# Kernel optimization log

Measured on AMD Instinct MI355X. Metric: run time of the kernel, lower is better.

The kernel has to match this reference:

```python
import jax, jax.numpy as jnp
import numpy as np

B, T, C, H = 4, 2048, 1024, 16
D = C // H          # head_dim = 64
FF = 2 * C          # ff_mult = 2
EPS = 1e-5


def _layernorm(x, g, b):
    mu = jnp.mean(x, axis=-1, keepdims=True)
    var = jnp.mean((x - mu) ** 2, axis=-1, keepdims=True)
    return (x - mu) * jax.lax.rsqrt(var + EPS) * g + b


def setup_inputs() -> dict:
    key = jax.random.key(0)
    ks = jax.random.split(key, 8)
    x = jax.random.normal(ks[0], (B, T, C), dtype=jnp.float32)
    perm = jax.random.permutation(ks[1], T).astype(jnp.int32)
    s_c = 1.0 / np.sqrt(C)
    s_f = 1.0 / np.sqrt(FF)
    Wqkv = jax.random.normal(ks[2], (C, 3 * C), dtype=jnp.float32) * s_c
    Wproj = jax.random.normal(ks[3], (C, C), dtype=jnp.float32) * s_c
    bproj = jnp.zeros((C,), dtype=jnp.float32)
    ln1_g = jnp.ones((C,), dtype=jnp.float32)
    ln1_b = jnp.zeros((C,), dtype=jnp.float32)
    ln2_g = jnp.ones((C,), dtype=jnp.float32)
    ln2_b = jnp.zeros((C,), dtype=jnp.float32)
    Wff1 = jax.random.normal(ks[4], (C, FF), dtype=jnp.float32) * s_c
    bff1 = jnp.zeros((FF,), dtype=jnp.float32)
    Wff2 = jax.random.normal(ks[5], (FF, C), dtype=jnp.float32) * s_f
    bff2 = jnp.zeros((C,), dtype=jnp.float32)
    return {"x": x, "perm": perm, "Wqkv": Wqkv, "Wproj": Wproj, "bproj": bproj,
            "ln1_g": ln1_g, "ln1_b": ln1_b, "ln2_g": ln2_g, "ln2_b": ln2_b,
            "Wff1": Wff1, "bff1": bff1, "Wff2": Wff2, "bff2": bff2}


def reference(x, perm, Wqkv, Wproj, bproj, ln1_g, ln1_b, ln2_g, ln2_b,
              Wff1, bff1, Wff2, bff2):
    # --- attention branch ---
    h = _layernorm(x, ln1_g, ln1_b)                       # [B,T,C]
    qkv = (h @ Wqkv).reshape(B, T, 3, H, D)
    q, k, v = qkv[:, :, 0], qkv[:, :, 1], qkv[:, :, 2]    # [B,T,H,D]
    # random-permuted causal additive mask: masked = ~tril[:, perm]
    rows = jnp.arange(T)[:, None]
    masked = perm[None, :] > rows                          # [T,T] bool
    bias = jnp.where(masked, -jnp.inf, 0.0).astype(x.dtype)
    scale = 1.0 / np.sqrt(D)
    scores = jnp.einsum('bqhd,bkhd->bhqk', q, k) * scale + bias
    attn = jax.nn.softmax(scores, axis=-1)                 # [B,H,T,T]
    y = jnp.einsum('bhqk,bkhd->bqhd', attn, v).reshape(B, T, C)
    x = x + y @ Wproj + bproj
    # --- MLP branch ---
    h2 = _layernorm(x, ln2_g, ln2_b)
    ff = jax.nn.gelu(h2 @ Wff1 + bff1, approximate=False) @ Wff2 + bff2
    return x + ff
```

## Files before the change

### kernel.cpp

```cpp
#include <hip/hip_runtime.h>
#include <math.h>

#define Bb 4
#define Tt 2048
#define Cc 1024
#define Hh 16
#define Dd 64
#define FFf 2048
#define Mrows (Bb*Tt)

typedef _Float16 f16;
typedef _Float16 half8 __attribute__((ext_vector_type(8)));
typedef _Float16 half4 __attribute__((ext_vector_type(4)));
typedef _Float16 half2 __attribute__((ext_vector_type(2)));
typedef float floatx4 __attribute__((ext_vector_type(4)));
typedef float floatx16 __attribute__((ext_vector_type(16)));

#define MFMA16(a,b,c)    __builtin_amdgcn_mfma_f32_16x16x32_f16(a,b,c,0,0,0)
#define MFMA16K16(a,b,c) __builtin_amdgcn_mfma_f32_16x16x16f16(a,b,c,0,0,0)
#define MFMA32(a,b,c)    __builtin_amdgcn_mfma_f32_32x32x16_f16(a,b,c,0,0,0)

__device__ __forceinline__ void g2l16(const void* g, void* l) {
  __builtin_amdgcn_global_load_lds((__attribute__((address_space(1))) void*)(g),
                                   (__attribute__((address_space(3))) void*)(l),
                                   16, 0, 0);
}

__device__ __forceinline__ float fast_gelu(float t) {
  const float z  = t * 0.70710678118654752f;
  const float az = fabsf(z);
  const float u  = __builtin_amdgcn_rcpf(1.0f + 0.3275911f * az);
  const float p  = u*(0.254829592f + u*(-0.284496736f + u*(1.421413741f +
                   u*(-1.453152027f + u*1.061405429f))));
  const float e  = 1.0f - p * __builtin_amdgcn_exp2f(-az*az*1.44269504089f);
  const float er = (z < 0.0f) ? -e : e;
  return 0.5f * t * (1.0f + er);
}

__global__ __launch_bounds__(256) void wt_ln_kernel(
    const float* __restrict__ Wqkv, const float* __restrict__ Wproj,
    const float* __restrict__ Wff1, const float* __restrict__ Wff2,
    f16* __restrict__ WqkvT, f16* __restrict__ WprojT,
    f16* __restrict__ Wff1T, f16* __restrict__ Wff2T,
    const float* __restrict__ x, const float* __restrict__ gam,
    const float* __restrict__ bet, f16* __restrict__ lnout,
    const int* __restrict__ perm, int* __restrict__ inv) {
  const int tid = threadIdx.x;
  if (blockIdx.x >= 16384) {
    #pragma unroll
    for (int i = tid; i < Tt; i += 256) inv[perm[i]] = i;
    return;
  }
  if (blockIdx.x < 8192) {
    __shared__ float tile[32][33];
    int idx = blockIdx.x;
    const float* W; f16* WT; int K, N, n0, k0;
    if (idx < 3072)      { W = Wqkv;  WT = WqkvT;  K = Cc;  N = 3*Cc; n0 = (idx % 96)*32; k0 = (idx / 96)*32; }
    else if (idx < 4096) { idx -= 3072; W = Wproj; WT = WprojT; K = Cc;  N = Cc;  n0 = (idx % 32)*32; k0 = (idx / 32)*32; }
    else if (idx < 6144) { idx -= 4096; W = Wff1;  WT = Wff1T;  K = Cc;  N = FFf; n0 = (idx % 64)*32; k0 = (idx / 64)*32; }
    else                 { idx -= 6144; W = Wff2;  WT = Wff2T;  K = FFf; N = Cc;  n0 = (idx % 32)*32; k0 = (idx / 32)*32; }
    const int tx = tid & 31, ty = tid >> 5;
    #pragma unroll
    for (int i = 0; i < 4; i++)
      tile[ty + 8*i][tx] = W[(size_t)(k0 + ty + 8*i) * N + n0 + tx];
    __syncthreads();
    #pragma unroll
    for (int i = 0; i < 4; i++)
      WT[(size_t)(n0 + ty + 8*i) * K + k0 + tx] = (f16)tile[tx][ty + 8*i];
  } else {
    const int row = blockIdx.x - 8192;
    const float4 v = ((const float4*)(x + (size_t)row * Cc))[tid];
    float s  = v.x + v.y + v.z + v.w;
    float ss = v.x*v.x + v.y*v.y + v.z*v.z + v.w*v.w;
    #pragma unroll
    for (int o = 32; o >= 1; o >>= 1) { s += __shfl_xor(s, o); ss += __shfl_xor(ss, o); }
    __shared__ float ps[4], pss[4];
    if ((tid & 63) == 0) { ps[tid >> 6] = s; pss[tid >> 6] = ss; }
    __syncthreads();
    s  = ps[0] + ps[1] + ps[2] + ps[3];
    ss = pss[0] + pss[1] + pss[2] + pss[3];
    const float mu   = s * (1.0f / Cc);
    const float rstd = rsqrtf(ss * (1.0f / Cc) - mu * mu + 1e-5f);
    const float4 g4 = ((const float4*)gam)[tid];
    const float4 b4 = ((const float4*)bet)[tid];
    half4 o;
    o[0] = (f16)((v.x - mu) * rstd * g4.x + b4.x);
    o[1] = (f16)((v.y - mu) * rstd * g4.y + b4.y);
    o[2] = (f16)((v.z - mu) * rstd * g4.z + b4.z);
    o[3] = (f16)((v.w - mu) * rstd * g4.w + b4.w);
    ((half4*)(lnout + (size_t)row * Cc))[tid] = o;
  }
}

__global__ __launch_bounds__(256) void ln_kernel(const float* __restrict__ x,
                                                 const float* __restrict__ gam,
                                                 const float* __restrict__ bet,
                                                 f16* __restrict__ out) {
  const int row = blockIdx.x;
  const int tid = threadIdx.x;
  const float4 v = ((const float4*)(x + (size_t)row * Cc))[tid];
  float s  = v.x + v.y + v.z + v.w;
  float ss = v.x*v.x + v.y*v.y + v.z*v.z + v.w*v.w;
  #pragma unroll
  for (int o = 32; o >= 1; o >>= 1) { s += __shfl_xor(s, o); ss += __shfl_xor(ss, o); }
  __shared__ float ps[4], pss[4];
  if ((tid & 63) == 0) { ps[tid >> 6] = s; pss[tid >> 6] = ss; }
  __syncthreads();
  s  = ps[0] + ps[1] + ps[2] + ps[3];
  ss = pss[0] + pss[1] + pss[2] + pss[3];
  const float mu   = s * (1.0f / Cc);
  const float rstd = rsqrtf(ss * (1.0f / Cc) - mu * mu + 1e-5f);
  const float4 g4 = ((const float4*)gam)[tid];
  const float4 b4 = ((const float4*)bet)[tid];
  half4 o;
  o[0] = (f16)((v.x - mu) * rstd * g4.x + b4.x);
  o[1] = (f16)((v.y - mu) * rstd * g4.y + b4.y);
  o[2] = (f16)((v.z - mu) * rstd * g4.z + b4.z);
  o[3] = (f16)((v.w - mu) * rstd * g4.w + b4.w);
  ((half4*)(out + (size_t)row * Cc))[tid] = o;
}

template <int MODE>
__device__ __forceinline__ void gemm_epilogue_tile(
    const floatx16& a, int rowBase, int col, int khalf,
    const float* __restrict__ resid, const float* __restrict__ bias,
    float* __restrict__ outF, f16* __restrict__ outH,
    f16* __restrict__ outQ, f16* __restrict__ outK, f16* __restrict__ outV) {
  if (MODE == 0) {
    const int s = col >> 10;
    const int hh = (col >> 6) & 15;
    const int d = col & 63;
    #pragma unroll
    for (int g = 0; g < 4; g++) {
      const int row0 = rowBase + 4*khalf + 8*g;
      const int bI = row0 >> 11;
      const int t0 = row0 & 2047;
      if (s == 2) {
        const size_t addr = (((size_t)(bI*Hh + hh)) * Dd + d) * Tt +
                            (t0 & ~63) + ((t0 >> 2) & 3)*16 + ((t0 >> 4) & 3)*4;
        half4 o;
        #pragma unroll
        for (int r = 0; r < 4; r++) o[r] = (f16)a[g*4 + r];
        *(half4*)&outV[addr] = o;
      } else {
        f16* dst = (s == 0) ? outQ : outK;
        const float sc = (s == 0) ? 0.18033688f : 1.0f;
        #pragma unroll
        for (int r = 0; r < 4; r++)
          dst[(((size_t)(bI*Hh + hh)) * Tt + t0 + r) * Dd + d] = (f16)(a[g*4 + r] * sc);
      }
    }
  } else {
    #pragma unroll
    for (int g = 0; g < 4; g++) {
      #pragma unroll
      for (int r = 0; r < 4; r++) {
        const int row = rowBase + 4*khalf + 8*g + r;
        const float vv = a[g*4 + r];
        if (MODE == 1) {
          const size_t ad = (size_t)row * Cc + col;
          outF[ad] = vv + resid[ad] + bias[col];
        } else if (MODE == 2) {
          outH[(size_t)row * FFf + col] = (f16)fast_gelu(vv + bias[col]);
        } else {
          const size_t ad = (size_t)row * Cc + col;
          outF[ad] = vv + bias[col] + resid[ad];
        }
      }
    }
  }
}

template <int MODE>
__global__ __launch_bounds__(256, 4) void gemm_kernel(
    const f16* __restrict__ A, const f16* __restrict__ Bt, const int Kdim,
    const float* __restrict__ resid, const float* __restrict__ bias,
    float* __restrict__ outF, f16* __restrict__ outH,
    f16* __restrict__ outQ, f16* __restrict__ outK, f16* __restrict__ outV,
    const int* __restrict__ inv) {
  __shared__ f16 As[128 * 64];
  __shared__ f16 Bs[128 * 64];
  const int tid = threadIdx.x;
  const int lane = tid & 63;
  const int w = tid >> 6;
  const int wr = w >> 1, wc = w & 1;

  const int fid = blockIdx.y * gridDim.x + blockIdx.x;
  const int xcd = fid & 7;
  const int s = fid >> 3;
  const int r = s & 63;
  const int bm = xcd * 8 + (r >> 3);
  const int bn = (s >> 6) * 8 + (r & 7);

  floatx16 acc[2][2] = {};

  const int srow = lane >> 3;
  const int scol = ((lane & 7) ^ srow) * 8;
  size_t aRow[4];
  {
    const int r0 = bm*128 + w*32 + srow;
    if (MODE == 0 && bn >= 8) {
      const int bI = r0 >> 11;
      const int t0 = r0 & 2047;
      #pragma unroll
      for (int c = 0; c < 4; c++)
        aRow[c] = (size_t)(bI*Tt + inv[t0 + c*8]) * Kdim + scol;
    } else {
      #pragma unroll
      for (int c = 0; c < 4; c++)
        aRow[c] = (size_t)(r0 + c*8) * Kdim + scol;
    }
  }
  const size_t bBase = (size_t)(bn*128 + w*32 + srow) * Kdim + scol;

  const int m0 = wr*64 + (lane & 31);
  const int n0 = wc*64 + (lane & 31);
  const int khalf = lane >> 5;
  const int mx = (lane & 7);

  for (int ks = 0; ks < Kdim; ks += 64) {
    __syncthreads();
    #pragma unroll
    for (int c = 0; c < 4; c++) {
      g2l16(A  + aRow[c] + ks, &As[(w*32 + c*8) * 64]);
      g2l16(Bt + bBase + (size_t)(c*8)*Kdim + ks, &Bs[(w*32 + c*8) * 64]);
    }
    __syncthreads();
    #pragma unroll
    for (int kk = 0; kk < 4; kk++) {
      const int kg = kk*2 + khalf;
      half8 aF[2], bF[2];
      aF[0] = *(const half8*)&As[(m0     ) * 64 + ((kg ^ mx) * 8)];
      aF[1] = *(const half8*)&As[(m0 + 32) * 64 + ((kg ^ mx) * 8)];
      bF[0] = *(const half8*)&Bs[(n0     ) * 64 + ((kg ^ mx) * 8)];
      bF[1] = *(const half8*)&Bs[(n0 + 32) * 64 + ((kg ^ mx) * 8)];
      acc[0][0] = MFMA32(aF[0], bF[0], acc[0][0]);
      acc[0][1] = MFMA32(aF[0], bF[1], acc[0][1]);
      acc[1][0] = MFMA32(aF[1], bF[0], acc[1][0]);
      acc[1][1] = MFMA32(aF[1], bF[1], acc[1][1]);
    }
  }

  #pragma unroll
  for (int mi = 0; mi < 2; mi++)
    #pragma unroll
    for (int ni = 0; ni < 2; ni++)
      gemm_epilogue_tile<MODE>(acc[mi][ni], bm*128 + wr*64 + mi*32,
                               bn*128 + wc*64 + ni*32 + (lane & 31), khalf,
                               resid, bias, outF, outH, outQ, outK, outV);
}

__global__ __launch_bounds__(512, 4) void attn_kernel(
    const f16* __restrict__ Q, const f16* __restrict__ Kg,
    const f16* __restrict__ Vtp, f16* __restrict__ Y) {
  __shared__ f16 Ks[2][64 * 64];
  __shared__ f16 Vs[2][64 * 64];

  const int tid = threadIdx.x;
  const int lane = tid & 63;
  const int w = tid >> 6;
  const int low = lane & 15;
  const int quad = lane >> 4;
  const int bh = blockIdx.x;
  const int y = blockIdx.y;
  const int b = bh >> 4, h = bh & 15;

  const half4 ones4 = {(f16)1.f, (f16)1.f, (f16)1.f, (f16)1.f};
  const int gd = ((lane & 7) ^ (lane >> 3)) * 8;
  const int krow = lane >> 3;
  const size_t kgB = (size_t)bh * Tt * Dd + (size_t)(w*8 + krow) * Dd + gd;
  const size_t vgB = (size_t)bh * Dd * Tt + (size_t)(w*8 + krow) * Tt + gd;

  for (int pi = 0; pi < 2; pi++) {
    const int tile = (pi == 0) ? y : 15 - y;
    const int q0 = tile * 128;

    half8 qF[2];
    {
      const size_t base = ((size_t)bh * Tt + q0 + w*16) * Dd;
      #pragma unroll
      for (int kc = 0; kc < 2; kc++)
        qF[kc] = *(const half8*)(Q + base + (size_t)low * Dd + kc*32 + quad*8);
    }

    floatx4 O[4] = {};
    floatx4 Ol = {};
    const int nkb = (q0 >> 6) + 2;

    g2l16(Kg  + kgB, &Ks[0][w * 512]);
    g2l16(Vtp + vgB, &Vs[0][w * 512]);
    __syncthreads();

    for (int kt = 0; kt < nkb; kt++) {
      const int cur = kt & 1;
      const int kbase = kt * 64;
      if (kt + 1 < nkb) {
        g2l16(Kg  + kgB + (size_t)(kbase + 64) * Dd, &Ks[cur ^ 1][w * 512]);
        g2l16(Vtp + vgB + (kbase + 64),              &Vs[cur ^ 1][w * 512]);
      }
      const f16* Kc = &Ks[cur][0];
      const f16* Vc = &Vs[cur][0];

      floatx4 S[4] = {};
      #pragma unroll
      for (int kc = 0; kc < 2; kc++) {
        #pragma unroll
        for (int ki = 0; ki < 4; ki++) {
          const int key = ki*16 + low;
          const half8 kf = *(const half8*)&Kc[key * 64 + (((kc*4 + quad) ^ (lane & 7)) * 8)];
          S[ki] = MFMA16(kf, qF[kc], S[ki]);
        }
      }

      half4 pF[4];
      const bool needmask = (kbase + 63 > q0 + w*16);
      if (needmask) {
        const int qrow = q0 + w*16 + low;
        #pragma unroll
        for (int ki = 0; ki < 4; ki++) {
          const floatx4 sv = S[ki];
          const int kj = kbase + ki*16 + quad*4;
          const float p0 = (kj + 0 > qrow) ? 0.f : __builtin_amdgcn_exp2f(sv[0]);
          const float p1 = (kj + 1 > qrow) ? 0.f : __builtin_amdgcn_exp2f(sv[1]);
          const float p2 = (kj + 2 > qrow) ? 0.f : __builtin_amdgcn_exp2f(sv[2]);
          const float p3 = (kj + 3 > qrow) ? 0.f : __builtin_amdgcn_exp2f(sv[3]);
          const half2 lo = __builtin_bit_cast(half2, __builtin_amdgcn_cvt_pkrtz(p0, p1));
          const half2 hi = __builtin_bit_cast(half2, __builtin_amdgcn_cvt_pkrtz(p2, p3));
          pF[ki] = __builtin_shufflevector(lo, hi, 0, 1, 2, 3);
        }
      } else {
        #pragma unroll
        for (int ki = 0; ki < 4; ki++) {
          const floatx4 sv = S[ki];
          const float p0 = __builtin_amdgcn_exp2f(sv[0]);
          const float p1 = __builtin_amdgcn_exp2f(sv[1]);
          const float p2 = __builtin_amdgcn_exp2f(sv[2]);
          const float p3 = __builtin_amdgcn_exp2f(sv[3]);
          const half2 lo = __builtin_bit_cast(half2, __builtin_amdgcn_cvt_pkrtz(p0, p1));
          const half2 hi = __builtin_bit_cast(half2, __builtin_amdgcn_cvt_pkrtz(p2, p3));
          pF[ki] = __builtin_shufflevector(lo, hi, 0, 1, 2, 3);
        }
      }

      #pragma unroll
      for (int ki2 = 0; ki2 < 2; ki2++) {
        Ol = MFMA16K16(ones4, pF[2*ki2 + 0], Ol);
        Ol = MFMA16K16(ones4, pF[2*ki2 + 1], Ol);
        #pragma unroll
        for (int ni = 0; ni < 4; ni++) {
          const int d = ni*16 + low;
          const half8 v8 = *(const half8*)&Vc[d * 64 + (((quad*2 + ki2) ^ (lane & 7)) * 8)];
          const half4 vfA = __builtin_shufflevector(v8, v8, 0, 1, 2, 3);
          const half4 vfB = __builtin_shufflevector(v8, v8, 4, 5, 6, 7);
          O[ni] = MFMA16K16(vfA, pF[2*ki2 + 0], O[ni]);
          O[ni] = MFMA16K16(vfB, pF[2*ki2 + 1], O[ni]);
        }
      }
      __syncthreads();
    }

    {
      const float linv = 1.0f / Ol[0];
      const int trow = q0 + w*16 + low;
      #pragma unroll
      for (int ni = 0; ni < 4; ni++) {
        half4 o;
        #pragma unroll
        for (int rr = 0; rr < 4; rr++) o[rr] = (f16)(O[ni][rr] * linv);
        *(half4*)&Y[((size_t)(b * Tt + trow)) * Cc + h*64 + ni*16 + quad*4] = o;
      }
    }
  }
}

extern "C" void kernel_launch(void* const* d_in, const int* in_sizes, int n_in,
                              void* d_out, int out_size, void* d_ws, size_t ws_size,
                              hipStream_t stream) {
  const float* x     = (const float*)d_in[0];
  const int*   perm  = (const int*)d_in[1];
  const float* Wqkv  = (const float*)d_in[2];
  const float* Wproj = (const float*)d_in[3];
  const float* bproj = (const float*)d_in[4];
  const float* ln1g  = (const float*)d_in[5];
  const float* ln1b  = (const float*)d_in[6];
  const float* ln2g  = (const float*)d_in[7];
  const float* ln2b  = (const float*)d_in[8];
  const float* Wff1  = (const float*)d_in[9];
  const float* bff1  = (const float*)d_in[10];
  const float* Wff2  = (const float*)d_in[11];
  const float* bff2  = (const float*)d_in[12];
  float* out = (float*)d_out;

  char* ws = (char*)d_ws;
  size_t off = 0;
  auto alloc = [&](size_t bytes) -> void* {
    void* p = ws + off;
    off += (bytes + 255) & ~(size_t)255;
    return p;
  };
  f16*   h1     = (f16*)alloc((size_t)Mrows * Cc * 2);
  f16*   qb     = (f16*)alloc((size_t)Mrows * Cc * 2);
  f16*   kb     = (f16*)alloc((size_t)Mrows * Cc * 2);
  f16*   vtp    = (f16*)alloc((size_t)Mrows * Cc * 2);
  f16*   yb     = (f16*)alloc((size_t)Mrows * Cc * 2);
  float* xa     = (float*)alloc((size_t)Mrows * Cc * 4);
  f16*   h2     = (f16*)alloc((size_t)Mrows * Cc * 2);
  f16*   gb     = (f16*)alloc((size_t)Mrows * FFf * 2);
  f16*   WqkvT  = (f16*)alloc((size_t)3 * Cc * Cc * 2);
  f16*   WprojT = (f16*)alloc((size_t)Cc * Cc * 2);
  f16*   Wff1T  = (f16*)alloc((size_t)FFf * Cc * 2);
  f16*   Wff2T  = (f16*)alloc((size_t)Cc * FFf * 2);
  int*   inv    = (int*)alloc((size_t)Tt * 4);

  wt_ln_kernel<<<16385, 256, 0, stream>>>(Wqkv, Wproj, Wff1, Wff2,
                                          WqkvT, WprojT, Wff1T, Wff2T,
                                          x, ln1g, ln1b, h1, perm, inv);

  gemm_kernel<0><<<dim3(3*Cc/128, Mrows/128), 256, 0, stream>>>(
      h1, WqkvT, Cc, nullptr, nullptr, nullptr, nullptr, qb, kb, vtp, inv);

  attn_kernel<<<dim3(Bb*Hh, Tt/256), 512, 0, stream>>>(qb, kb, vtp, yb);

  gemm_kernel<1><<<dim3(Cc/128, Mrows/128), 256, 0, stream>>>(
      yb, WprojT, Cc, x, bproj, xa, nullptr, nullptr, nullptr, nullptr, nullptr);

  ln_kernel<<<Mrows, 256, 0, stream>>>(xa, ln2g, ln2b, h2);

  gemm_kernel<2><<<dim3(FFf/128, Mrows/128), 256, 0, stream>>>(
      h2, Wff1T, Cc, nullptr, bff1, nullptr, gb, nullptr, nullptr, nullptr, nullptr);

  gemm_kernel<3><<<dim3(Cc/128, Mrows/128), 256, 0, stream>>>(
      gb, Wff2T, FFf, xa, bff2, out, nullptr, nullptr, nullptr, nullptr, nullptr);
}
```

Before: 388.3 us.

## Double-buffer LDS staging in projection GEMMs and raise wave priority around attention MFMAs

For GEMM modes 1 and 3, the kernel now allocates two LDS buffers for A and B. The next K tile is prefetched with global_load_lds while the current tile is computed, and the loop uses one barrier per iteration instead of two. The attention kernel wraps its QK and PV MFMA sections in s_setprio(1)/s_setprio(0) so matrix work gets issue priority over other waves. Doubling LDS in those GEMM modes may lower occupancy under the 4-blocks-per-CU launch bound.

```diff
diff --git a/kernel.cpp b/kernel.cpp
--- a/kernel.cpp
+++ b/kernel.cpp
@@ -178,8 +178,9 @@
     float* __restrict__ outF, f16* __restrict__ outH,
     f16* __restrict__ outQ, f16* __restrict__ outK, f16* __restrict__ outV,
     const int* __restrict__ inv) {
-  __shared__ f16 As[128 * 64];
-  __shared__ f16 Bs[128 * 64];
+  constexpr int NB = (MODE == 1 || MODE == 3) ? 2 : 1;
+  __shared__ f16 As[NB][128 * 64];
+  __shared__ f16 Bs[NB][128 * 64];
   const int tid = threadIdx.x;
   const int lane = tid & 63;
   const int w = tid >> 6;
@@ -218,26 +219,45 @@
   const int khalf = lane >> 5;
   const int mx = (lane & 7);
 
-  for (int ks = 0; ks < Kdim; ks += 64) {
-    __syncthreads();
+  auto stage = [&](int buf, int ks) {
     #pragma unroll
     for (int c = 0; c < 4; c++) {
-      g2l16(A  + aRow[c] + ks, &As[(w*32 + c*8) * 64]);
-      g2l16(Bt + bBase + (size_t)(c*8)*Kdim + ks, &Bs[(w*32 + c*8) * 64]);
-    }
-    __syncthreads();
+      g2l16(A  + aRow[c] + ks, &As[buf][(w*32 + c*8) * 64]);
+      g2l16(Bt + bBase + (size_t)(c*8)*Kdim + ks, &Bs[buf][(w*32 + c*8) * 64]);
+    }
+  };
+  auto compute = [&](int buf) {
     #pragma unroll
     for (int kk = 0; kk < 4; kk++) {
       const int kg = kk*2 + khalf;
       half8 aF[2], bF[2];
-      aF[0] = *(const half8*)&As[(m0     ) * 64 + ((kg ^ mx) * 8)];
-      aF[1] = *(const half8*)&As[(m0 + 32) * 64 + ((kg ^ mx) * 8)];
-      bF[0] = *(const half8*)&Bs[(n0     ) * 64 + ((kg ^ mx) * 8)];
-      bF[1] = *(const half8*)&Bs[(n0 + 32) * 64 + ((kg ^ mx) * 8)];
+      aF[0] = *(const half8*)&As[buf][(m0     ) * 64 + ((kg ^ mx) * 8)];
+      aF[1] = *(const half8*)&As[buf][(m0 + 32) * 64 + ((kg ^ mx) * 8)];
+      bF[0] = *(const half8*)&Bs[buf][(n0     ) * 64 + ((kg ^ mx) * 8)];
+      bF[1] = *(const half8*)&Bs[buf][(n0 + 32) * 64 + ((kg ^ mx) * 8)];
       acc[0][0] = MFMA32(aF[0], bF[0], acc[0][0]);
       acc[0][1] = MFMA32(aF[0], bF[1], acc[0][1]);
       acc[1][0] = MFMA32(aF[1], bF[0], acc[1][0]);
       acc[1][1] = MFMA32(aF[1], bF[1], acc[1][1]);
+    }
+  };
+
+  if constexpr (NB == 2) {
+    stage(0, 0);
+    __syncthreads();
+    const int NT = Kdim >> 6;
+    for (int t = 0; t < NT; ++t) {
+      const int cur = t & 1;
+      if (t + 1 < NT) stage(cur ^ 1, (t + 1) << 6);
+      compute(cur);
+      __syncthreads();
+    }
+  } else {
+    for (int ks = 0; ks < Kdim; ks += 64) {
+      __syncthreads();
+      stage(0, ks);
+      __syncthreads();
+      compute(0);
     }
   }
 
@@ -302,6 +322,7 @@
       const f16* Vc = &Vs[cur][0];
 
       floatx4 S[4] = {};
+      __builtin_amdgcn_s_setprio(1);
       #pragma unroll
       for (int kc = 0; kc < 2; kc++) {
         #pragma unroll
@@ -311,6 +332,7 @@
           S[ki] = MFMA16(kf, qF[kc], S[ki]);
         }
       }
+      __builtin_amdgcn_s_setprio(0);
 
       half4 pF[4];
       const bool needmask = (kbase + 63 > q0 + w*16);
@@ -342,6 +364,7 @@
         }
       }
 
+      __builtin_amdgcn_s_setprio(1);
       #pragma unroll
       for (int ki2 = 0; ki2 < 2; ki2++) {
         Ol = MFMA16K16(ones4, pF[2*ki2 + 0], Ol);
@@ -356,6 +379,7 @@
           O[ni] = MFMA16K16(vfB, pF[2*ki2 + 1], O[ni]);
         }
       }
+      __builtin_amdgcn_s_setprio(0);
       __syncthreads();
     }
 
```

After: 372.3 us. 4.1% less time.
